# Optimization experiments

Hardware: AMD Instinct MI355X
Metric: run time of the kernel (lower is better)

The kernel has to match this reference:

```python
import jax, jax.numpy as jnp
import numpy as np

VOCAB_SIZE = 13
EMBED_DIM = 50
HIDDEN_DIM = 50
BATCH = 2048
SEQ_LEN = 2048


def setup_inputs() -> dict:
    key = jax.random.key(0)
    ks = jax.random.split(key, 10)
    s = 0.1
    return {
        "x": jax.random.randint(ks[0], (BATCH, SEQ_LEN), 0, VOCAB_SIZE),
        "embed": jax.random.normal(ks[1], (VOCAB_SIZE, EMBED_DIM), jnp.float32),
        "W_ih": jax.random.normal(ks[2], (4 * HIDDEN_DIM, EMBED_DIM), jnp.float32) * s,
        "W_hh": jax.random.normal(ks[3], (4 * HIDDEN_DIM, HIDDEN_DIM), jnp.float32) * s,
        "b_ih": jax.random.normal(ks[4], (4 * HIDDEN_DIM,), jnp.float32) * s,
        "b_hh": jax.random.normal(ks[5], (4 * HIDDEN_DIM,), jnp.float32) * s,
        "W1": jax.random.normal(ks[6], (HIDDEN_DIM, HIDDEN_DIM), jnp.float32) * s,
        "b1": jax.random.normal(ks[7], (HIDDEN_DIM,), jnp.float32) * s,
        "W2": jax.random.normal(ks[8], (1, HIDDEN_DIM), jnp.float32) * s,
        "b2": jax.random.normal(ks[9], (1,), jnp.float32) * s,
    }


def reference(x, embed, W_ih, W_hh, b_ih, b_hh, W1, b1, W2, b2):
    B = x.shape[0]
    H = HIDDEN_DIM
    embeds = embed[x]                    # [B, T, E]
    xs = jnp.swapaxes(embeds, 0, 1)      # [T, B, E] for scan over time

    def step(carry, xt):
        hx, cx = carry
        gates = xt @ W_ih.T + b_ih + hx @ W_hh.T + b_hh   # [B, 4H]
        i = jax.nn.sigmoid(gates[:, 0 * H:1 * H])
        f = jax.nn.sigmoid(gates[:, 1 * H:2 * H])
        g = jnp.tanh(gates[:, 2 * H:3 * H])
        o = jax.nn.sigmoid(gates[:, 3 * H:4 * H])
        cx = f * cx + i * g
        hx = o * jnp.tanh(cx)
        return (hx, cx), None

    init = (jnp.zeros((B, H), embeds.dtype), jnp.zeros((B, H), embeds.dtype))
    (hx, _), _ = jax.lax.scan(step, init, xs)

    h = jax.nn.relu(hx @ W1.T + b1)
    out = (h @ W2.T + b2).squeeze(1)     # [B]
    return out
```

## Files before the change

### kernel.cpp

```cpp
#include <hip/hip_runtime.h>
#include <hip/hip_fp16.h>

#define T_SEQ 2048
#define HID   50
#define KP    64
#define MB    4
#define NBLK  512
#define NTHR  256
#define HSTR  80
#define BUFB  (MB*HSTR)

typedef __attribute__((ext_vector_type(8))) _Float16 half8;
typedef __attribute__((ext_vector_type(4))) float    f32x4;

__device__ __forceinline__ ushort f16b(float f){ return __half_as_ushort(__float2half(f)); }
__device__ __forceinline__ float rcp_(float x){ return __builtin_amdgcn_rcpf(x); }
__device__ __forceinline__ float sigm(float x){ return rcp_(1.f + __expf(-x)); }
__device__ __forceinline__ float tanh_(float x){ return fmaf(2.f, rcp_(1.f + __expf(-2.f*x)), -1.f); }
__device__ __forceinline__ float sel4(int q, float a, float b, float c, float d){
    float x = (q == 0) ? a : b;
    float y = (q == 2) ? c : d;
    return (q < 2) ? x : y;
}

__global__ void build_B(const float* __restrict__ embed, const float* __restrict__ Wih,
                        const float* __restrict__ Whh, const float* __restrict__ bih,
                        const float* __restrict__ bhh, ushort* __restrict__ Bm) {
    int idx = blockIdx.x * blockDim.x + threadIdx.x;
    if (idx >= 256 * KP) return;
    int col = idx >> 6, k = idx & 63;
    int wq = col >> 6, g = (col >> 4) & 3, cc = col & 15;
    int u = wq * 16 + cc;
    ushort v = 0;
    if (u < HID) {
        int r = g * HID + u;
        if (k < HID) {
            v = f16b(Whh[r * HID + k]);
        } else if (k < 63) {
            float s = 0.f;
            for (int e = 0; e < HID; ++e)
                s = fmaf(embed[(k - 50) * HID + e], Wih[r * HID + e], s);
            v = f16b(s);
        } else {
            v = f16b(bih[r] + bhh[r]);
        }
    }
    Bm[idx] = v;
}

__global__ __launch_bounds__(NTHR, 2) void lstm4(
    const int*    __restrict__ x,
    const ushort* __restrict__ Bm,
    const float*  __restrict__ W1,
    const float*  __restrict__ b1,
    const float*  __restrict__ W2,
    const float*  __restrict__ b2,
    float*        __restrict__ out)
{
    const int t   = threadIdx.x;
    const int w   = t >> 6;
    const int l   = t & 63;
    const int q   = l >> 4;
    const int c16 = l & 15;
    const int u   = w * 16 + c16;

    __shared__ __align__(16) ushort hbuf[2 * BUFB];
    __shared__ float zb[HID * MB];

    half8 bf[4][2];
    {
        const ushort* bp = Bm + (w * 64 + c16) * KP + q * 8;
        #pragma unroll
        for (int j = 0; j < 4; ++j) {
            bf[j][0] = *(const half8*)(bp + j * 16 * KP);
            bf[j][1] = *(const half8*)(bp + j * 16 * KP + 32);
        }
    }
    #pragma unroll
    for (int j = 0; j < 4; ++j)
        asm volatile("" : "+v"(bf[j][0]), "+v"(bf[j][1]));

    for (int i = t; i < 2 * BUFB; i += NTHR) hbuf[i] = 0;

    const int  row0 = blockIdx.x * MB;
    const long xb   = (long)row0 * T_SEQ;
    int t0r = 0, t1r = 0, t2r = 0;
    __syncthreads();
    if (t < MB) {
        int tk0 = x[xb + (long)t * T_SEQ + 0];
        int tk1 = x[xb + (long)t * T_SEQ + 1];
        hbuf[0 * BUFB + t * HSTR + 63] = 0x3C00;
        hbuf[1 * BUFB + t * HSTR + 63] = 0x3C00;
        hbuf[0 * BUFB + t * HSTR + 50 + tk0] = 0x3C00;
        hbuf[1 * BUFB + t * HSTR + 50 + tk1] = 0x3C00;
        t0r = tk1; t1r = tk0; t2r = tk1;
    }
    __syncthreads();

    const ushort* ar  = hbuf + (c16 & 3) * HSTR + q * 8;
    ushort*       wr_ = hbuf + q * HSTR + u;

    float cst = 0.f;

#define STEP(P) do {                                                              \
        int pf = 0;                                                               \
        if (t < MB) {                                                             \
            int it = step + 2 + (P); if (it > T_SEQ - 1) it = T_SEQ - 1;          \
            pf = x[xb + (long)t * T_SEQ + it];                                    \
        }                                                                         \
        half8 a0 = *(const half8*)(ar + (P) * BUFB);                              \
        half8 a1 = *(const half8*)(ar + (P) * BUFB + 32);                         \
        const f32x4 zz = {0.f, 0.f, 0.f, 0.f};                                    \
        f32x4 z0 = __builtin_amdgcn_mfma_f32_16x16x32_f16(a0, bf[0][0], zz,0,0,0);\
        z0 = __builtin_amdgcn_mfma_f32_16x16x32_f16(a1, bf[0][1], z0, 0,0,0);     \
        f32x4 z1 = __builtin_amdgcn_mfma_f32_16x16x32_f16(a0, bf[1][0], zz,0,0,0);\
        z1 = __builtin_amdgcn_mfma_f32_16x16x32_f16(a1, bf[1][1], z1, 0,0,0);     \
        f32x4 z2 = __builtin_amdgcn_mfma_f32_16x16x32_f16(a0, bf[2][0], zz,0,0,0);\
        z2 = __builtin_amdgcn_mfma_f32_16x16x32_f16(a1, bf[2][1], z2, 0,0,0);     \
        f32x4 z3 = __builtin_amdgcn_mfma_f32_16x16x32_f16(a0, bf[3][0], zz,0,0,0);\
        z3 = __builtin_amdgcn_mfma_f32_16x16x32_f16(a1, bf[3][1], z3, 0,0,0);     \
        float gi = sel4(q, z0[0], z0[1], z0[2], z0[3]);                           \
        float gf = sel4(q, z1[0], z1[1], z1[2], z1[3]);                           \
        float gg = sel4(q, z2[0], z2[1], z2[2], z2[3]);                           \
        float go = sel4(q, z3[0], z3[1], z3[2], z3[3]);                           \
        float iv = sigm(gi), fv = sigm(gf), gv = tanh_(gg), ov = sigm(go);        \
        cst = fmaf(fv, cst, iv * gv);                                             \
        float hh = ov * tanh_(cst);                                               \
        if (u < HID) wr_[(1 - (P)) * BUFB] = f16b(hh);                            \
        if (t < MB) {                                                             \
            ushort* hb = hbuf + (1 - (P)) * BUFB + t * HSTR + 50;                 \
            hb[t0r] = 0;                                                          \
            hb[t2r] = 0x3C00;                                                     \
            t0r = t1r; t1r = t2r; t2r = pf;                                       \
        }                                                                         \
        __syncthreads();                                                          \
    } while (0)

    #pragma unroll 1
    for (int step = 0; step < T_SEQ; step += 2) {
        STEP(0);
        STEP(1);
    }
#undef STEP

    if (t < MB * HID) {
        int m = t & 3, uu = t >> 2;
        float a = b1[uu];
        const ushort* hr = hbuf + m * HSTR;
        #pragma unroll 10
        for (int k = 0; k < HID; ++k)
            a = fmaf(W1[uu * HID + k], __half2float(__ushort_as_half(hr[k])), a);
        zb[uu * MB + m] = fmaxf(a, 0.f);
    }
    __syncthreads();
    if (t < MB) {
        float a = b2[0];
        #pragma unroll 10
        for (int j = 0; j < HID; ++j)
            a = fmaf(W2[j], zb[j * MB + t], a);
        out[row0 + t] = a;
    }
}

extern "C" void kernel_launch(void* const* d_in, const int* in_sizes, int n_in,
                              void* d_out, int out_size, void* d_ws, size_t ws_size,
                              hipStream_t stream) {
    const int*   x     = (const int*)  d_in[0];
    const float* embed = (const float*)d_in[1];
    const float* W_ih  = (const float*)d_in[2];
    const float* W_hh  = (const float*)d_in[3];
    const float* b_ih  = (const float*)d_in[4];
    const float* b_hh  = (const float*)d_in[5];
    const float* W1    = (const float*)d_in[6];
    const float* b1    = (const float*)d_in[7];
    const float* W2    = (const float*)d_in[8];
    const float* b2    = (const float*)d_in[9];
    float* out = (float*)d_out;

    ushort* Bm = (ushort*)d_ws;

    build_B<<<(256 * KP + NTHR - 1) / NTHR, NTHR, 0, stream>>>(
        embed, W_ih, W_hh, b_ih, b_hh, Bm);

    lstm4<<<NBLK, NTHR, 0, stream>>>(
        x, Bm, W1, b1, W2, b2, out);
}
```

Before: 773.6 us.

## Process eight batch rows per block to fill more of each MFMA tile

Each block now handles 8 sequences instead of 4, using 8 of the 16 MFMA rows rather than 4. Every lane computes two hidden-unit cells per step, so the grid is halved to 256 blocks and launch bounds drop to one block per SIMD set. This amortises the serial per-step MFMA, barrier and LDS latency over twice the rows. The cost is more VALU transcendental work per lane and fewer resident blocks for hiding latency.

```diff
diff --git a/kernel.cpp b/kernel.cpp
--- a/kernel.cpp
+++ b/kernel.cpp
@@ -4,8 +4,8 @@
 #define T_SEQ 2048
 #define HID   50
 #define KP    64
-#define MB    4
-#define NBLK  512
+#define MB    8
+#define NBLK  256
 #define NTHR  256
 #define HSTR  80
 #define BUFB  (MB*HSTR)
@@ -17,11 +17,6 @@
 __device__ __forceinline__ float rcp_(float x){ return __builtin_amdgcn_rcpf(x); }
 __device__ __forceinline__ float sigm(float x){ return rcp_(1.f + __expf(-x)); }
 __device__ __forceinline__ float tanh_(float x){ return fmaf(2.f, rcp_(1.f + __expf(-2.f*x)), -1.f); }
-__device__ __forceinline__ float sel4(int q, float a, float b, float c, float d){
-    float x = (q == 0) ? a : b;
-    float y = (q == 2) ? c : d;
-    return (q < 2) ? x : y;
-}
 
 __global__ void build_B(const float* __restrict__ embed, const float* __restrict__ Wih,
                         const float* __restrict__ Whh, const float* __restrict__ bih,
@@ -48,7 +43,7 @@
     Bm[idx] = v;
 }
 
-__global__ __launch_bounds__(NTHR, 2) void lstm4(
+__global__ __launch_bounds__(NTHR, 1) void lstm8(
     const int*    __restrict__ x,
     const ushort* __restrict__ Bm,
     const float*  __restrict__ W1,
@@ -63,6 +58,7 @@
     const int q   = l >> 4;
     const int c16 = l & 15;
     const int u   = w * 16 + c16;
+    const int r0  = (q & 2) + 4 * (q & 1);
 
     __shared__ __align__(16) ushort hbuf[2 * BUFB];
     __shared__ float zb[HID * MB];
@@ -97,10 +93,10 @@
     }
     __syncthreads();
 
-    const ushort* ar  = hbuf + (c16 & 3) * HSTR + q * 8;
-    ushort*       wr_ = hbuf + q * HSTR + u;
+    const ushort* ar  = hbuf + (c16 & 7) * HSTR + q * 8;
+    ushort*       wr_ = hbuf + r0 * HSTR + u;
 
-    float cst = 0.f;
+    float c0 = 0.f, c1 = 0.f;
 
 #define STEP(P) do {                                                              \
         int pf = 0;                                                               \
@@ -111,22 +107,29 @@
         half8 a0 = *(const half8*)(ar + (P) * BUFB);                              \
         half8 a1 = *(const half8*)(ar + (P) * BUFB + 32);                         \
         const f32x4 zz = {0.f, 0.f, 0.f, 0.f};                                    \
+        f32x4 z1 = __builtin_amdgcn_mfma_f32_16x16x32_f16(a0, bf[1][0], zz,0,0,0);\
+        z1 = __builtin_amdgcn_mfma_f32_16x16x32_f16(a1, bf[1][1], z1, 0,0,0);     \
         f32x4 z0 = __builtin_amdgcn_mfma_f32_16x16x32_f16(a0, bf[0][0], zz,0,0,0);\
         z0 = __builtin_amdgcn_mfma_f32_16x16x32_f16(a1, bf[0][1], z0, 0,0,0);     \
-        f32x4 z1 = __builtin_amdgcn_mfma_f32_16x16x32_f16(a0, bf[1][0], zz,0,0,0);\
-        z1 = __builtin_amdgcn_mfma_f32_16x16x32_f16(a1, bf[1][1], z1, 0,0,0);     \
         f32x4 z2 = __builtin_amdgcn_mfma_f32_16x16x32_f16(a0, bf[2][0], zz,0,0,0);\
         z2 = __builtin_amdgcn_mfma_f32_16x16x32_f16(a1, bf[2][1], z2, 0,0,0);     \
         f32x4 z3 = __builtin_amdgcn_mfma_f32_16x16x32_f16(a0, bf[3][0], zz,0,0,0);\
         z3 = __builtin_amdgcn_mfma_f32_16x16x32_f16(a1, bf[3][1], z3, 0,0,0);     \
-        float gi = sel4(q, z0[0], z0[1], z0[2], z0[3]);                           \
-        float gf = sel4(q, z1[0], z1[1], z1[2], z1[3]);                           \
-        float gg = sel4(q, z2[0], z2[1], z2[2], z2[3]);                           \
-        float go = sel4(q, z3[0], z3[1], z3[2], z3[3]);                           \
-        float iv = sigm(gi), fv = sigm(gf), gv = tanh_(gg), ov = sigm(go);        \
-        cst = fmaf(fv, cst, iv * gv);                                             \
-        float hh = ov * tanh_(cst);                                               \
-        if (u < HID) wr_[(1 - (P)) * BUFB] = f16b(hh);                            \
+        bool hi = (q & 2) != 0;                                                   \
+        float vf_a = hi ? z1[2] : z1[0], vf_b = hi ? z1[3] : z1[1];               \
+        float vi_a = hi ? z0[2] : z0[0], vi_b = hi ? z0[3] : z0[1];               \
+        float vg_a = hi ? z2[2] : z2[0], vg_b = hi ? z2[3] : z2[1];               \
+        float vo_a = hi ? z3[2] : z3[0], vo_b = hi ? z3[3] : z3[1];               \
+        float f0 = sigm(vf_a), i0 = sigm(vi_a), g0 = tanh_(vg_a), o0 = sigm(vo_a);\
+        float f1 = sigm(vf_b), i1 = sigm(vi_b), g1 = tanh_(vg_b), o1 = sigm(vo_b);\
+        c0 = fmaf(f0, c0, i0 * g0);                                               \
+        c1 = fmaf(f1, c1, i1 * g1);                                               \
+        float h0 = o0 * tanh_(c0);                                                \
+        float h1 = o1 * tanh_(c1);                                                \
+        if (u < HID) {                                                            \
+            wr_[(1 - (P)) * BUFB] = f16b(h0);                                     \
+            wr_[(1 - (P)) * BUFB + HSTR] = f16b(h1);                              \
+        }                                                                         \
         if (t < MB) {                                                             \
             ushort* hb = hbuf + (1 - (P)) * BUFB + t * HSTR + 50;                 \
             hb[t0r] = 0;                                                          \
@@ -143,8 +146,8 @@
     }
 #undef STEP
 
-    if (t < MB * HID) {
-        int m = t & 3, uu = t >> 2;
+    for (int idx = t; idx < MB * HID; idx += NTHR) {
+        int m = idx & 7, uu = idx >> 3;
         float a = b1[uu];
         const ushort* hr = hbuf + m * HSTR;
         #pragma unroll 10
@@ -182,6 +185,6 @@
     build_B<<<(256 * KP + NTHR - 1) / NTHR, NTHR, 0, stream>>>(
         embed, W_ih, W_hh, b_ih, b_hh, Bm);
 
-    lstm4<<<NBLK, NTHR, 0, stream>>>(
+    lstm8<<<NBLK, NTHR, 0, stream>>>(
         x, Bm, W1, b1, W2, b2, out);
 }
```

Result: slower. 803.7 us (+3.9%).

## Fold log2e scaling into weights and merge gate reciprocals in LSTM step

Applied to the files above, without the earlier changes.

Pre-scales the recurrent, embedding and bias weights by -log2(e), or -2log2(e) for the cell gate, so gates feed exp2 directly. The i, f and g activations now share one reciprocal, and the output gate and tanh(c) share another. The A-row mapping changes to c16>>2, so each lane reads z[0] directly and the per-gate select is gone. It also adds s_setprio around the MFMAs and spreads the token one-hot updates so one lane per wave handles its own row. This shortens the serial per-step dependency chain, at the cost of clamped exponent inputs and products of large terms that could cost precision.

```diff
diff --git a/kernel.cpp b/kernel.cpp
--- a/kernel.cpp
+++ b/kernel.cpp
@@ -10,18 +10,15 @@
 #define HSTR  80
 #define BUFB  (MB*HSTR)
 
+#define NLOG2E  1.4426950408889634f
+#define N2LOG2E 2.8853900817779268f
+
 typedef __attribute__((ext_vector_type(8))) _Float16 half8;
 typedef __attribute__((ext_vector_type(4))) float    f32x4;
 
 __device__ __forceinline__ ushort f16b(float f){ return __half_as_ushort(__float2half(f)); }
 __device__ __forceinline__ float rcp_(float x){ return __builtin_amdgcn_rcpf(x); }
-__device__ __forceinline__ float sigm(float x){ return rcp_(1.f + __expf(-x)); }
-__device__ __forceinline__ float tanh_(float x){ return fmaf(2.f, rcp_(1.f + __expf(-2.f*x)), -1.f); }
-__device__ __forceinline__ float sel4(int q, float a, float b, float c, float d){
-    float x = (q == 0) ? a : b;
-    float y = (q == 2) ? c : d;
-    return (q < 2) ? x : y;
-}
+__device__ __forceinline__ float ex2_(float x){ return __builtin_amdgcn_exp2f(x); }
 
 __global__ void build_B(const float* __restrict__ embed, const float* __restrict__ Wih,
                         const float* __restrict__ Whh, const float* __restrict__ bih,
@@ -34,15 +31,16 @@
     ushort v = 0;
     if (u < HID) {
         int r = g * HID + u;
+        float s = (g == 2) ? -N2LOG2E : -NLOG2E;
         if (k < HID) {
-            v = f16b(Whh[r * HID + k]);
+            v = f16b(s * Whh[r * HID + k]);
         } else if (k < 63) {
-            float s = 0.f;
+            float t = 0.f;
             for (int e = 0; e < HID; ++e)
-                s = fmaf(embed[(k - 50) * HID + e], Wih[r * HID + e], s);
-            v = f16b(s);
+                t = fmaf(embed[(k - 50) * HID + e], Wih[r * HID + e], t);
+            v = f16b(s * t);
         } else {
-            v = f16b(bih[r] + bhh[r]);
+            v = f16b(s * (bih[r] + bhh[r]));
         }
     }
     Bm[idx] = v;
@@ -86,31 +84,32 @@
     const long xb   = (long)row0 * T_SEQ;
     int t0r = 0, t1r = 0, t2r = 0;
     __syncthreads();
-    if (t < MB) {
-        int tk0 = x[xb + (long)t * T_SEQ + 0];
-        int tk1 = x[xb + (long)t * T_SEQ + 1];
-        hbuf[0 * BUFB + t * HSTR + 63] = 0x3C00;
-        hbuf[1 * BUFB + t * HSTR + 63] = 0x3C00;
-        hbuf[0 * BUFB + t * HSTR + 50 + tk0] = 0x3C00;
-        hbuf[1 * BUFB + t * HSTR + 50 + tk1] = 0x3C00;
+    if (l == 0) {
+        int tk0 = x[xb + (long)w * T_SEQ + 0];
+        int tk1 = x[xb + (long)w * T_SEQ + 1];
+        hbuf[0 * BUFB + w * HSTR + 63] = 0x3C00;
+        hbuf[1 * BUFB + w * HSTR + 63] = 0x3C00;
+        hbuf[0 * BUFB + w * HSTR + 50 + tk0] = 0x3C00;
+        hbuf[1 * BUFB + w * HSTR + 50 + tk1] = 0x3C00;
         t0r = tk1; t1r = tk0; t2r = tk1;
     }
     __syncthreads();
 
-    const ushort* ar  = hbuf + (c16 & 3) * HSTR + q * 8;
+    const ushort* ar  = hbuf + (c16 >> 2) * HSTR + q * 8;
     ushort*       wr_ = hbuf + q * HSTR + u;
 
     float cst = 0.f;
 
 #define STEP(P) do {                                                              \
-        int pf = 0;                                                               \
-        if (t < MB) {                                                             \
+        int tknf = 0;                                                             \
+        if (l == 0) {                                                             \
             int it = step + 2 + (P); if (it > T_SEQ - 1) it = T_SEQ - 1;          \
-            pf = x[xb + (long)t * T_SEQ + it];                                    \
+            tknf = x[xb + (long)w * T_SEQ + it];                                  \
         }                                                                         \
         half8 a0 = *(const half8*)(ar + (P) * BUFB);                              \
         half8 a1 = *(const half8*)(ar + (P) * BUFB + 32);                         \
         const f32x4 zz = {0.f, 0.f, 0.f, 0.f};                                    \
+        __builtin_amdgcn_s_setprio(1);                                            \
         f32x4 z0 = __builtin_amdgcn_mfma_f32_16x16x32_f16(a0, bf[0][0], zz,0,0,0);\
         z0 = __builtin_amdgcn_mfma_f32_16x16x32_f16(a1, bf[0][1], z0, 0,0,0);     \
         f32x4 z1 = __builtin_amdgcn_mfma_f32_16x16x32_f16(a0, bf[1][0], zz,0,0,0);\
@@ -119,19 +118,27 @@
         z2 = __builtin_amdgcn_mfma_f32_16x16x32_f16(a1, bf[2][1], z2, 0,0,0);     \
         f32x4 z3 = __builtin_amdgcn_mfma_f32_16x16x32_f16(a0, bf[3][0], zz,0,0,0);\
         z3 = __builtin_amdgcn_mfma_f32_16x16x32_f16(a1, bf[3][1], z3, 0,0,0);     \
-        float gi = sel4(q, z0[0], z0[1], z0[2], z0[3]);                           \
-        float gf = sel4(q, z1[0], z1[1], z1[2], z1[3]);                           \
-        float gg = sel4(q, z2[0], z2[1], z2[2], z2[3]);                           \
-        float go = sel4(q, z3[0], z3[1], z3[2], z3[3]);                           \
-        float iv = sigm(gi), fv = sigm(gf), gv = tanh_(gg), ov = sigm(go);        \
-        cst = fmaf(fv, cst, iv * gv);                                             \
-        float hh = ov * tanh_(cst);                                               \
+        __builtin_amdgcn_s_setprio(0);                                            \
+        \
+        float pi = ex2_(fminf(z0[0], 30.f));                          \
+        float pf = ex2_(fminf(z1[0], 30.f));                          \
+        float qg = ex2_(fminf(z2[0], 30.f));                          \
+        float Df = 1.f + pf;                                                      \
+        float D2 = (1.f + pi) * (1.f + qg);                                       \
+        float iv1 = rcp_(Df * D2);                                                \
+        float fv  = iv1 * D2;                                       \
+        float ig  = iv1 * Df * (1.f - qg);                 \
+        cst = fmaf(fv, cst, ig);                                                  \
+        float po = ex2_(fminf(z3[0], 30.f));                          \
+        float qc = ex2_(fminf(cst * -N2LOG2E, 30.f));                  \
+        float iv2 = rcp_((1.f + po) * (1.f + qc));                                \
+        float hh  = iv2 * (1.f - qc);                       \
         if (u < HID) wr_[(1 - (P)) * BUFB] = f16b(hh);                            \
-        if (t < MB) {                                                             \
-            ushort* hb = hbuf + (1 - (P)) * BUFB + t * HSTR + 50;                 \
+        if (l == 0) {                                                             \
+            ushort* hb = hbuf + (1 - (P)) * BUFB + w * HSTR + 50;                 \
             hb[t0r] = 0;                                                          \
             hb[t2r] = 0x3C00;                                                     \
-            t0r = t1r; t1r = t2r; t2r = pf;                                       \
+            t0r = t1r; t1r = t2r; t2r = tknf;                                     \
         }                                                                         \
         __syncthreads();                                                          \
     } while (0)
```

Result: faster. 707.6 us (-8.5%).
